# Performance work log

Measured on AMD Instinct MI355X. Metric: run time of the kernel, lower is better.

## Reference

```python
import jax, jax.numpy as jnp
import numpy as np

EPS = 1e-6
NEG_SLOPE = 0.2
B, C, E, F = 8, 2048, 256, 256


def setup_inputs() -> dict:
    key = jax.random.key(0)
    k1, k2, k3, k4, k5, k6 = jax.random.split(key, 6)
    X = jax.random.normal(k1, (B, C, E, 3), dtype=jnp.float32)
    J = jax.random.normal(k2, (B, C, E, 3), dtype=jnp.float32)
    A = jax.random.normal(k3, (F, E), dtype=jnp.float32)
    Bw = jax.random.normal(k4, (F, E), dtype=jnp.float32)
    Cw = jax.random.normal(k5, (F, E), dtype=jnp.float32)
    # VNLeakyReLU map_to_dir weight [F, F] (nn.Linear-style scale)
    W = jax.random.normal(k6, (F, F), dtype=jnp.float32) / jnp.sqrt(jnp.float32(F))
    return {"X": X, "J": J, "A": A, "Bw": Bw, "Cw": Cw, "W": W}


def _basis(J):
    # normalized direction [B,C,E,3]
    nJ = J / (jnp.linalg.norm(J, axis=-1, keepdims=True) + EPS)
    sub = nJ[..., :2]                                   # [B,C,E,2]
    Uz = -(sub * sub).sum(-1) / (nJ[..., 2] + EPS)      # [B,C,E]
    U = jnp.concatenate([sub, Uz[..., None]], axis=-1)  # [B,C,E,3]
    nU = U / (jnp.linalg.norm(U, axis=-1, keepdims=True) + EPS)
    nV = jnp.cross(nU, nJ)                              # [B,C,E,3]
    # rows of R are (U, V, J): R[..., i, j] matches torch reshape of cat
    return jnp.stack([nU, nV, nJ], axis=-2)             # [B,C,E,3,3]


def reference(X, J, A, Bw, Cw, W):
    R = _basis(J)                                        # [B,C,E,3,3]
    RT = jnp.swapaxes(R, -1, -2)                         # [B,C,E,3,3]
    # rtx[..., i] = RT[..., i, :] . X  (per torch get_rtx)
    rtx = jnp.einsum('bceij,bcej->bcei', RT, X)          # [B,C,E,3]

    def rrtx(i, r):
        # indexed_R = R[..., :, i]; broadcast-multiply by scalar field r
        return R[..., :, i] * r[..., None]               # [B,C,E,3]

    a = rrtx(0, rtx[..., 0]) + rrtx(1, rtx[..., 1])
    b = rrtx(1, rtx[..., 0]) - rrtx(0, rtx[..., 1])
    c = rrtx(2, rtx[..., 2])
    Y = (jnp.einsum('fe,bcei->bcfi', A, a)
         + jnp.einsum('fe,bcei->bcfi', Bw, b)
         + jnp.einsum('fe,bcei->bcfi', Cw, c))           # [B,C,F,3]

    x = jnp.transpose(Y, (0, 2, 3, 1))                   # [B,F,3,C]
    # VNLeakyReLU: direction d via linear over feature dim
    d = jnp.einsum('fg,bgic->bfic', W, x)                # [B,F,3,C]
    dot = (x * d).sum(axis=2, keepdims=True)             # [B,F,1,C]
    mask = (dot >= 0).astype(x.dtype)
    dns = (d * d).sum(axis=2, keepdims=True)
    x_out = (NEG_SLOPE * x
             + (1.0 - NEG_SLOPE) * (mask * x
                                    + (1.0 - mask) * (x - dot / (dns + EPS) * d)))
    return x_out
```

## Files before the change

### kernel.cpp

```cpp
#include <hip/hip_runtime.h>


constexpr float EPSf  = 1e-6f;
constexpr int Bdim = 8, Cdim = 2048, Edim = 256, Fdim = 256;
constexpr int NT  = 16;
constexpr int KC1 = 24;
constexpr int KC2 = 8;
constexpr int ZLD = 776;
constexpr int YLD = 264;
constexpr int M_ROWS = KC1 * 16 * 64;
constexpr int W_ROWS = KC2 * 16 * 64;

typedef __attribute__((ext_vector_type(8))) _Float16 half8;
typedef __attribute__((ext_vector_type(4))) _Float16 half4;
typedef __attribute__((ext_vector_type(4))) float    f32x4;

__device__ __forceinline__ void basis_abc(float Xx, float Xy, float Xz,
                                          float Jx, float Jy, float Jz,
                                          float* a, float* bb, float* cc)
{
    const float jn  = sqrtf(Jx*Jx + Jy*Jy + Jz*Jz) + EPSf;
    const float rj  = 1.0f / jn;
    const float nJx = Jx * rj, nJy = Jy * rj, nJz = Jz * rj;
    const float h   = nJx*nJx + nJy*nJy;
    const float Uz  = -h / (nJz + EPSf);
    const float un  = sqrtf(h + Uz*Uz) + EPSf;
    const float ru  = 1.0f / un;
    const float nUx = nJx * ru, nUy = nJy * ru, nUz = Uz * ru;
    const float nVx = nUy*nJz - nUz*nJy;
    const float nVy = nUz*nJx - nUx*nJz;
    const float nVz = nUx*nJy - nUy*nJx;
    const float r0 = nUx*Xx + nVx*Xy + nJx*Xz;
    const float r1 = nUy*Xx + nVy*Xy + nJy*Xz;
    const float r2 = nUz*Xx + nVz*Xy + nJz*Xz;
    a[0]  = nUx*r0 + nUy*r1;   a[1]  = nVx*r0 + nVy*r1;   a[2]  = nJx*r0 + nJy*r1;
    bb[0] = nUy*r0 - nUx*r1;   bb[1] = nVy*r0 - nVx*r1;   bb[2] = nJy*r0 - nJx*r1;
    cc[0] = nUz*r2;            cc[1] = nVz*r2;            cc[2] = nJz*r2;
}

__global__ __launch_bounds__(256)
void prep_weights_f16(const float* __restrict__ Ap, const float* __restrict__ Bp,
                      const float* __restrict__ Cp, const float* __restrict__ Wp,
                      _Float16* __restrict__ ws)
{
    const int tid = blockIdx.x * 256 + threadIdx.x;
    const bool isW = tid >= M_ROWS;
    const int row = isW ? tid - M_ROWS : tid;
    const int l   = row & 63;
    const int ft  = (row >> 6) & 15;
    const int kc  = row >> 10;
    const int f   = ft * 16 + (l & 15);
    const int k0  = kc * 32 + ((l >> 4) << 3);

    const float* src;
    int e0;
    if (isW)            { src = Wp; e0 = k0; }
    else if (k0 < 256)  { src = Ap; e0 = k0; }
    else if (k0 < 512)  { src = Bp; e0 = k0 - 256; }
    else                { src = Cp; e0 = k0 - 512; }

    const float* p = src + f * 256 + e0;
    half8 v;
    #pragma unroll
    for (int j = 0; j < 8; ++j) v[j] = (_Float16)p[j];

    _Float16* dst = ws + (isW ? (size_t)M_ROWS * 8 : 0);
    *reinterpret_cast<half8*>(dst + (size_t)row * 8) = v;
}

__global__ __launch_bounds__(512, 4)
void fused_mfma_f16(const float* __restrict__ Xp, const float* __restrict__ Jp,
                    const _Float16* __restrict__ wsM, const _Float16* __restrict__ wsW,
                    float* __restrict__ outp)
{
    __shared__ __align__(16) _Float16 lds[48 * ZLD];

    const int t  = threadIdx.x;
    const int s0 = blockIdx.x * NT;
    const int b  = s0 >> 11;
    const int c0 = s0 & (Cdim - 1);

    {
        const int equad = t & 63;
        const int sq    = t >> 6;
        const int e0    = equad * 4;
        #pragma unroll
        for (int ss = 0; ss < 2; ++ss) {
            const int s = sq * 2 + ss;
            const long site = (long)(b * Cdim + c0 + s);
            const float4* X4 = reinterpret_cast<const float4*>(Xp) + site * 192 + equad * 3;
            const float4* J4 = reinterpret_cast<const float4*>(Jp) + site * 192 + equad * 3;
            const float4 xA = X4[0], xB = X4[1], xC = X4[2];
            const float4 jA = J4[0], jB = J4[1], jC = J4[2];
            const float xf[12] = {xA.x,xA.y,xA.z,xA.w, xB.x,xB.y,xB.z,xB.w, xC.x,xC.y,xC.z,xC.w};
            const float jf[12] = {jA.x,jA.y,jA.z,jA.w, jB.x,jB.y,jB.z,jB.w, jC.x,jC.y,jC.z,jC.w};

            half4 za[3], zb[3], zc[3];
            #pragma unroll
            for (int ee = 0; ee < 4; ++ee) {
                float a[3], bb[3], cc[3];
                basis_abc(xf[3*ee], xf[3*ee+1], xf[3*ee+2],
                          jf[3*ee], jf[3*ee+1], jf[3*ee+2], a, bb, cc);
                #pragma unroll
                for (int i = 0; i < 3; ++i) {
                    za[i][ee] = (_Float16)a[i];
                    zb[i][ee] = (_Float16)bb[i];
                    zc[i][ee] = (_Float16)cc[i];
                }
            }
            #pragma unroll
            for (int i = 0; i < 3; ++i) {
                _Float16* rowp = &lds[(i * NT + s) * ZLD];
                *reinterpret_cast<half4*>(rowp +       e0) = za[i];
                *reinterpret_cast<half4*>(rowp + 256 + e0) = zb[i];
                *reinterpret_cast<half4*>(rowp + 512 + e0) = zc[i];
            }
        }
    }
    __syncthreads();

    const int wid = t >> 6;
    const int l   = t & 63;
    const int lr  = l & 15;
    const int lk  = (l >> 4) * 8;

    f32x4 Yacc[2][3];
    #pragma unroll
    for (int q = 0; q < 2; ++q)
        #pragma unroll
        for (int nt = 0; nt < 3; ++nt)
            Yacc[q][nt] = f32x4{0.f, 0.f, 0.f, 0.f};

    const half8* Mf = reinterpret_cast<const half8*>(wsM);
    for (int kc = 0; kc < KC1; ++kc) {
        half8 af[2];
        #pragma unroll
        for (int q = 0; q < 2; ++q)
            af[q] = Mf[(kc * 16 + wid * 2 + q) * 64 + l];
        half8 zf[3];
        #pragma unroll
        for (int nt = 0; nt < 3; ++nt)
            zf[nt] = *reinterpret_cast<const half8*>(&lds[(nt * NT + lr) * ZLD + kc * 32 + lk]);
        #pragma unroll
        for (int q = 0; q < 2; ++q)
            #pragma unroll
            for (int nt = 0; nt < 3; ++nt)
                Yacc[q][nt] = __builtin_amdgcn_mfma_f32_16x16x32_f16(af[q], zf[nt], Yacc[q][nt], 0, 0, 0);
    }
    __syncthreads();

    #pragma unroll
    for (int q = 0; q < 2; ++q) {
        const int row = (wid * 2 + q) * 16 + (l >> 4) * 4;
        #pragma unroll
        for (int nt = 0; nt < 3; ++nt) {
            const int col = nt * NT + lr;
            half4 v = { (_Float16)Yacc[q][nt][0], (_Float16)Yacc[q][nt][1],
                        (_Float16)Yacc[q][nt][2], (_Float16)Yacc[q][nt][3] };
            *reinterpret_cast<half4*>(&lds[col * YLD + row]) = v;
        }
    }
    __syncthreads();

    f32x4 Dacc[2][3];
    #pragma unroll
    for (int q = 0; q < 2; ++q)
        #pragma unroll
        for (int nt = 0; nt < 3; ++nt)
            Dacc[q][nt] = f32x4{0.f, 0.f, 0.f, 0.f};

    const half8* Wf = reinterpret_cast<const half8*>(wsW);
    for (int kc = 0; kc < KC2; ++kc) {
        half8 af[2];
        #pragma unroll
        for (int q = 0; q < 2; ++q)
            af[q] = Wf[(kc * 16 + wid * 2 + q) * 64 + l];
        half8 yf[3];
        #pragma unroll
        for (int nt = 0; nt < 3; ++nt)
            yf[nt] = *reinterpret_cast<const half8*>(&lds[(nt * NT + lr) * YLD + kc * 32 + lk]);
        #pragma unroll
        for (int q = 0; q < 2; ++q)
            #pragma unroll
            for (int nt = 0; nt < 3; ++nt)
                Dacc[q][nt] = __builtin_amdgcn_mfma_f32_16x16x32_f16(af[q], yf[nt], Dacc[q][nt], 0, 0, 0);
    }

    #pragma unroll
    for (int q = 0; q < 2; ++q) {
        const int fbase = (wid * 2 + q) * 16 + (l >> 4) * 4;
        #pragma unroll
        for (int r = 0; r < 4; ++r) {
#pragma clang fp contract(off)
            const float x0 = Yacc[q][0][r], x1 = Yacc[q][1][r], x2 = Yacc[q][2][r];
            const float d0 = Dacc[q][0][r], d1 = Dacc[q][1][r], d2 = Dacc[q][2][r];
            const float dot = (x0*d0 + x1*d1) + x2*d2;
            const float dns = (d0*d0 + d1*d1) + d2*d2;
            const float sc  = dot / (dns + EPSf);
            const bool  pos = (dot >= 0.f);
            const int f = fbase + r;
            const long obase = ((long)(b * Fdim + f) * 3) * Cdim + c0 + lr;
            const float c0v = pos ? x0 : (x0 - sc*d0);
            const float c1v = pos ? x1 : (x1 - sc*d1);
            const float c2v = pos ? x2 : (x2 - sc*d2);
            outp[obase + 0 * Cdim] = 0.2f*x0 + 0.8f*c0v;
            outp[obase + 1 * Cdim] = 0.2f*x1 + 0.8f*c1v;
            outp[obase + 2 * Cdim] = 0.2f*x2 + 0.8f*c2v;
        }
    }
}

__device__ __forceinline__ float comp(const float4& v, int k) {
    return k == 0 ? v.x : k == 1 ? v.y : k == 2 ? v.z : v.w;
}

__global__ __launch_bounds__(256)
void fused_cl_lrelu_fp32(const float* __restrict__ Xp, const float* __restrict__ Jp,
                         const float* __restrict__ Ap, const float* __restrict__ Bp,
                         const float* __restrict__ Cp, const float* __restrict__ Wp,
                         float* __restrict__ outp)
{
    __shared__ float4 sabc[4 * Edim * 3];
    __shared__ float  ylds[4 * 3][Fdim];

    const int t   = threadIdx.x;
    const int s0  = blockIdx.x * 4;
    const int b   = s0 / Cdim;
    const int c0  = s0 % Cdim;

    #pragma unroll
    for (int r = 0; r < 4; ++r) {
        const int e  = t;
        const int idx = ((b * Cdim + c0 + r) * Edim + e) * 3;
        float a[3], bb[3], cc[3];
        basis_abc(Xp[idx], Xp[idx+1], Xp[idx+2], Jp[idx], Jp[idx+1], Jp[idx+2], a, bb, cc);
        const int base = (r * Edim + e) * 3;
        sabc[base + 0] = make_float4(a[0], a[1], a[2], bb[0]);
        sabc[base + 1] = make_float4(bb[1], bb[2], cc[0], cc[1]);
        sabc[base + 2] = make_float4(cc[2], 0.f, 0.f, 0.f);
    }
    __syncthreads();

    const int fl = t & 63;
    const int cg = t >> 6;
    float Y[4][3];
    #pragma unroll
    for (int q = 0; q < 4; ++q) Y[q][0] = Y[q][1] = Y[q][2] = 0.f;

    const float4* A4 = reinterpret_cast<const float4*>(Ap);
    const float4* B4 = reinterpret_cast<const float4*>(Bp);
    const float4* C4 = reinterpret_cast<const float4*>(Cp);
    for (int e4 = 0; e4 < Edim / 4; ++e4) {
        float4 wa[4], wb[4], wc[4];
        #pragma unroll
        for (int q = 0; q < 4; ++q) {
            const int f = q * 64 + fl;
            wa[q] = A4[f * (Edim/4) + e4];
            wb[q] = B4[f * (Edim/4) + e4];
            wc[q] = C4[f * (Edim/4) + e4];
        }
        #pragma unroll
        for (int k = 0; k < 4; ++k) {
            const int e = e4 * 4 + k;
            const float4 p0 = sabc[(cg * Edim + e) * 3 + 0];
            const float4 p1 = sabc[(cg * Edim + e) * 3 + 1];
            const float4 p2 = sabc[(cg * Edim + e) * 3 + 2];
            #pragma unroll
            for (int q = 0; q < 4; ++q) {
                const float Af = comp(wa[q], k), Bf = comp(wb[q], k), Cf = comp(wc[q], k);
                Y[q][0] += Af * p0.x + Bf * p0.w + Cf * p1.z;
                Y[q][1] += Af * p0.y + Bf * p1.x + Cf * p1.w;
                Y[q][2] += Af * p0.z + Bf * p1.y + Cf * p2.x;
            }
        }
    }
    #pragma unroll
    for (int q = 0; q < 4; ++q) {
        const int f = q * 64 + fl;
        ylds[cg * 3 + 0][f] = Y[q][0];
        ylds[cg * 3 + 1][f] = Y[q][1];
        ylds[cg * 3 + 2][f] = Y[q][2];
    }
    __syncthreads();

    float D[4][3];
    #pragma unroll
    for (int q = 0; q < 4; ++q) D[q][0] = D[q][1] = D[q][2] = 0.f;
    const float4* W4 = reinterpret_cast<const float4*>(Wp);
    for (int g4 = 0; g4 < Fdim / 4; ++g4) {
        float4 ww[4];
        #pragma unroll
        for (int q = 0; q < 4; ++q) ww[q] = W4[(q * 64 + fl) * (Fdim/4) + g4];
        const float4 y0 = *reinterpret_cast<const float4*>(&ylds[cg * 3 + 0][g4 * 4]);
        const float4 y1 = *reinterpret_cast<const float4*>(&ylds[cg * 3 + 1][g4 * 4]);
        const float4 y2 = *reinterpret_cast<const float4*>(&ylds[cg * 3 + 2][g4 * 4]);
        #pragma unroll
        for (int k = 0; k < 4; ++k) {
            #pragma unroll
            for (int q = 0; q < 4; ++q) {
                const float Wv = comp(ww[q], k);
                D[q][0] += Wv * comp(y0, k);
                D[q][1] += Wv * comp(y1, k);
                D[q][2] += Wv * comp(y2, k);
            }
        }
    }

    float* outl = reinterpret_cast<float*>(sabc);
    #pragma unroll
    for (int q = 0; q < 4; ++q) {
        const int f = q * 64 + fl;
        const float dot = (Y[q][0]*D[q][0] + Y[q][1]*D[q][1]) + Y[q][2]*D[q][2];
        const float dns = (D[q][0]*D[q][0] + D[q][1]*D[q][1]) + D[q][2]*D[q][2];
        const float s   = dot / (dns + EPSf);
        const bool  pos = (dot >= 0.f);
        #pragma unroll
        for (int i = 0; i < 3; ++i) {
            const float x = Y[q][i], d = D[q][i];
            outl[(f * 3 + i) * 4 + cg] = 0.2f*x + 0.8f*(pos ? x : x - s*d);
        }
    }
    __syncthreads();
    const float4* o4 = reinterpret_cast<const float4*>(outl);
    float4* O4 = reinterpret_cast<float4*>(outp);
    const int c4 = c0 >> 2;
    #pragma unroll
    for (int i = 0; i < 3; ++i)
        O4[((b * Fdim + t) * 3 + i) * (Cdim / 4) + c4] = o4[t * 3 + i];
}

extern "C" void kernel_launch(void* const* d_in, const int* in_sizes, int n_in,
                              void* d_out, int out_size, void* d_ws, size_t ws_size,
                              hipStream_t stream) {
    const float* X  = (const float*)d_in[0];
    const float* J  = (const float*)d_in[1];
    const float* A  = (const float*)d_in[2];
    const float* Bw = (const float*)d_in[3];
    const float* Cw = (const float*)d_in[4];
    const float* W  = (const float*)d_in[5];
    float* out = (float*)d_out;

    constexpr size_t WS_NEED = (size_t)(M_ROWS + W_ROWS) * 8 * sizeof(_Float16);
    if (ws_size >= WS_NEED) {
        _Float16* wsM = (_Float16*)d_ws;
        _Float16* wsW = wsM + (size_t)M_ROWS * 8;
        prep_weights_f16<<<(M_ROWS + W_ROWS) / 256, 256, 0, stream>>>(A, Bw, Cw, W, wsM);
        fused_mfma_f16<<<Bdim * Cdim / NT, 512, 0, stream>>>(X, J, wsM, wsW, out);
    } else {
        fused_cl_lrelu_fp32<<<Bdim * Cdim / 4, 256, 0, stream>>>(X, J, A, Bw, Cw, W, out);
    }
}
```

Baseline: 60.40 us.

## Persist blocks over four site groups with double-buffered basis prefetch

Each block now processes four 16-site groups in sequence with 1024 threads (16 waves, one 16-row F tile per wave instead of two). The next group's X/J are loaded into registers during the current group's GEMMs, and its basis values are written into the alternate LDS buffer after the epilogue. The aim is to hide global load latency behind MFMA work and cut the number of blocks launched. In exchange, LDS use doubles, each wave gets less MFMA work per weight fragment load, and the large block size may reduce occupancy.

```diff
diff --git a/kernel.cpp b/kernel.cpp
--- a/kernel.cpp
+++ b/kernel.cpp
@@ -8,6 +8,8 @@
 constexpr int KC2 = 8;
 constexpr int ZLD = 776;
 constexpr int YLD = 264;
+constexpr int ZSZ = 48 * ZLD;
+constexpr int GROUPS = 4;
 constexpr int M_ROWS = KC1 * 16 * 64;
 constexpr int W_ROWS = KC2 * 16 * 64;
 
@@ -68,145 +70,146 @@
     *reinterpret_cast<half8*>(dst + (size_t)row * 8) = v;
 }
 
-__global__ __launch_bounds__(512, 4)
+__global__ __launch_bounds__(1024, 4)
 void fused_mfma_f16(const float* __restrict__ Xp, const float* __restrict__ Jp,
                     const _Float16* __restrict__ wsM, const _Float16* __restrict__ wsW,
                     float* __restrict__ outp)
 {
-    __shared__ __align__(16) _Float16 lds[48 * ZLD];
-
-    const int t  = threadIdx.x;
-    const int s0 = blockIdx.x * NT;
-    const int b  = s0 >> 11;
-    const int c0 = s0 & (Cdim - 1);
-
-    {
-        const int equad = t & 63;
-        const int sq    = t >> 6;
-        const int e0    = equad * 4;
-        #pragma unroll
-        for (int ss = 0; ss < 2; ++ss) {
-            const int s = sq * 2 + ss;
-            const long site = (long)(b * Cdim + c0 + s);
-            const float4* X4 = reinterpret_cast<const float4*>(Xp) + site * 192 + equad * 3;
-            const float4* J4 = reinterpret_cast<const float4*>(Jp) + site * 192 + equad * 3;
-            const float4 xA = X4[0], xB = X4[1], xC = X4[2];
-            const float4 jA = J4[0], jB = J4[1], jC = J4[2];
-            const float xf[12] = {xA.x,xA.y,xA.z,xA.w, xB.x,xB.y,xB.z,xB.w, xC.x,xC.y,xC.z,xC.w};
-            const float jf[12] = {jA.x,jA.y,jA.z,jA.w, jB.x,jB.y,jB.z,jB.w, jC.x,jC.y,jC.z,jC.w};
-
-            half4 za[3], zb[3], zc[3];
-            #pragma unroll
-            for (int ee = 0; ee < 4; ++ee) {
-                float a[3], bb[3], cc[3];
-                basis_abc(xf[3*ee], xf[3*ee+1], xf[3*ee+2],
-                          jf[3*ee], jf[3*ee+1], jf[3*ee+2], a, bb, cc);
-                #pragma unroll
-                for (int i = 0; i < 3; ++i) {
-                    za[i][ee] = (_Float16)a[i];
-                    zb[i][ee] = (_Float16)bb[i];
-                    zc[i][ee] = (_Float16)cc[i];
-                }
-            }
+    __shared__ __align__(16) _Float16 lds[2 * ZSZ];
+
+    const int t     = threadIdx.x;
+    const int site  = t >> 6;
+    const int equad = t & 63;
+    const int e0    = equad * 4;
+    const int wid   = site;
+    const int l     = t & 63;
+    const int lr    = l & 15;
+    const int lk    = (l >> 4) * 8;
+    const int g0    = blockIdx.x * GROUPS;
+
+    float4 xv[3], jv[3];
+
+    auto LOADIN = [&](int g) {
+        const long sg = (long)(g0 + g) * NT + site;
+        const float4* X4 = reinterpret_cast<const float4*>(Xp) + sg * 192 + equad * 3;
+        const float4* J4 = reinterpret_cast<const float4*>(Jp) + sg * 192 + equad * 3;
+        xv[0] = X4[0]; xv[1] = X4[1]; xv[2] = X4[2];
+        jv[0] = J4[0]; jv[1] = J4[1]; jv[2] = J4[2];
+    };
+
+    auto BASIS_STORE = [&](int g) {
+        _Float16* Z = lds + (g & 1) * ZSZ;
+        const float xf[12] = {xv[0].x,xv[0].y,xv[0].z,xv[0].w,
+                              xv[1].x,xv[1].y,xv[1].z,xv[1].w,
+                              xv[2].x,xv[2].y,xv[2].z,xv[2].w};
+        const float jf[12] = {jv[0].x,jv[0].y,jv[0].z,jv[0].w,
+                              jv[1].x,jv[1].y,jv[1].z,jv[1].w,
+                              jv[2].x,jv[2].y,jv[2].z,jv[2].w};
+        half4 za[3], zb[3], zc[3];
+        #pragma unroll
+        for (int ee = 0; ee < 4; ++ee) {
+            float a[3], bb[3], cc[3];
+            basis_abc(xf[3*ee], xf[3*ee+1], xf[3*ee+2],
+                      jf[3*ee], jf[3*ee+1], jf[3*ee+2], a, bb, cc);
             #pragma unroll
             for (int i = 0; i < 3; ++i) {
-                _Float16* rowp = &lds[(i * NT + s) * ZLD];
-                *reinterpret_cast<half4*>(rowp +       e0) = za[i];
-                *reinterpret_cast<half4*>(rowp + 256 + e0) = zb[i];
-                *reinterpret_cast<half4*>(rowp + 512 + e0) = zc[i];
-            }
-        }
-    }
+                za[i][ee] = (_Float16)a[i];
+                zb[i][ee] = (_Float16)bb[i];
+                zc[i][ee] = (_Float16)cc[i];
+            }
+        }
+        #pragma unroll
+        for (int i = 0; i < 3; ++i) {
+            _Float16* rowp = Z + (i * NT + site) * ZLD;
+            *reinterpret_cast<half4*>(rowp +       e0) = za[i];
+            *reinterpret_cast<half4*>(rowp + 256 + e0) = zb[i];
+            *reinterpret_cast<half4*>(rowp + 512 + e0) = zc[i];
+        }
+    };
+
+    LOADIN(0);
+    BASIS_STORE(0);
     __syncthreads();
 
-    const int wid = t >> 6;
-    const int l   = t & 63;
-    const int lr  = l & 15;
-    const int lk  = (l >> 4) * 8;
-
-    f32x4 Yacc[2][3];
-    #pragma unroll
-    for (int q = 0; q < 2; ++q)
-        #pragma unroll
-        for (int nt = 0; nt < 3; ++nt)
-            Yacc[q][nt] = f32x4{0.f, 0.f, 0.f, 0.f};
-
     const half8* Mf = reinterpret_cast<const half8*>(wsM);
-    for (int kc = 0; kc < KC1; ++kc) {
-        half8 af[2];
-        #pragma unroll
-        for (int q = 0; q < 2; ++q)
-            af[q] = Mf[(kc * 16 + wid * 2 + q) * 64 + l];
-        half8 zf[3];
-        #pragma unroll
-        for (int nt = 0; nt < 3; ++nt)
-            zf[nt] = *reinterpret_cast<const half8*>(&lds[(nt * NT + lr) * ZLD + kc * 32 + lk]);
-        #pragma unroll
-        for (int q = 0; q < 2; ++q)
+    const half8* Wf = reinterpret_cast<const half8*>(wsW);
+
+    for (int g = 0; g < GROUPS; ++g) {
+        const _Float16* Z = lds + (g & 1) * ZSZ;
+
+        if (g + 1 < GROUPS) LOADIN(g + 1);
+
+        f32x4 Yacc[3];
+        #pragma unroll
+        for (int nt = 0; nt < 3; ++nt) Yacc[nt] = f32x4{0.f, 0.f, 0.f, 0.f};
+
+        for (int kc = 0; kc < KC1; ++kc) {
+            half8 af = Mf[(kc * 16 + wid) * 64 + l];
+            half8 zf[3];
             #pragma unroll
             for (int nt = 0; nt < 3; ++nt)
-                Yacc[q][nt] = __builtin_amdgcn_mfma_f32_16x16x32_f16(af[q], zf[nt], Yacc[q][nt], 0, 0, 0);
-    }
-    __syncthreads();
-
-    #pragma unroll
-    for (int q = 0; q < 2; ++q) {
-        const int row = (wid * 2 + q) * 16 + (l >> 4) * 4;
-        #pragma unroll
-        for (int nt = 0; nt < 3; ++nt) {
-            const int col = nt * NT + lr;
-            half4 v = { (_Float16)Yacc[q][nt][0], (_Float16)Yacc[q][nt][1],
-                        (_Float16)Yacc[q][nt][2], (_Float16)Yacc[q][nt][3] };
-            *reinterpret_cast<half4*>(&lds[col * YLD + row]) = v;
-        }
-    }
-    __syncthreads();
-
-    f32x4 Dacc[2][3];
-    #pragma unroll
-    for (int q = 0; q < 2; ++q)
-        #pragma unroll
-        for (int nt = 0; nt < 3; ++nt)
-            Dacc[q][nt] = f32x4{0.f, 0.f, 0.f, 0.f};
-
-    const half8* Wf = reinterpret_cast<const half8*>(wsW);
-    for (int kc = 0; kc < KC2; ++kc) {
-        half8 af[2];
-        #pragma unroll
-        for (int q = 0; q < 2; ++q)
-            af[q] = Wf[(kc * 16 + wid * 2 + q) * 64 + l];
-        half8 yf[3];
-        #pragma unroll
-        for (int nt = 0; nt < 3; ++nt)
-            yf[nt] = *reinterpret_cast<const half8*>(&lds[(nt * NT + lr) * YLD + kc * 32 + lk]);
-        #pragma unroll
-        for (int q = 0; q < 2; ++q)
+                zf[nt] = *reinterpret_cast<const half8*>(&Z[(nt * NT + lr) * ZLD + kc * 32 + lk]);
             #pragma unroll
             for (int nt = 0; nt < 3; ++nt)
-                Dacc[q][nt] = __builtin_amdgcn_mfma_f32_16x16x32_f16(af[q], yf[nt], Dacc[q][nt], 0, 0, 0);
-    }
-
-    #pragma unroll
-    for (int q = 0; q < 2; ++q) {
-        const int fbase = (wid * 2 + q) * 16 + (l >> 4) * 4;
-        #pragma unroll
-        for (int r = 0; r < 4; ++r) {
+                Yacc[nt] = __builtin_amdgcn_mfma_f32_16x16x32_f16(af, zf[nt], Yacc[nt], 0, 0, 0);
+        }
+        __syncthreads();
+
+        _Float16* Yt = lds + (g & 1) * ZSZ;
+        {
+            const int row = wid * 16 + (l >> 4) * 4;
+            #pragma unroll
+            for (int nt = 0; nt < 3; ++nt) {
+                const int col = nt * NT + lr;
+                half4 v = { (_Float16)Yacc[nt][0], (_Float16)Yacc[nt][1],
+                            (_Float16)Yacc[nt][2], (_Float16)Yacc[nt][3] };
+                *reinterpret_cast<half4*>(&Yt[col * YLD + row]) = v;
+            }
+        }
+        __syncthreads();
+
+        f32x4 Dacc[3];
+        #pragma unroll
+        for (int nt = 0; nt < 3; ++nt) Dacc[nt] = f32x4{0.f, 0.f, 0.f, 0.f};
+
+        for (int kc = 0; kc < KC2; ++kc) {
+            half8 wf = Wf[(kc * 16 + wid) * 64 + l];
+            half8 yf[3];
+            #pragma unroll
+            for (int nt = 0; nt < 3; ++nt)
+                yf[nt] = *reinterpret_cast<const half8*>(&Yt[(nt * NT + lr) * YLD + kc * 32 + lk]);
+            #pragma unroll
+            for (int nt = 0; nt < 3; ++nt)
+                Dacc[nt] = __builtin_amdgcn_mfma_f32_16x16x32_f16(wf, yf[nt], Dacc[nt], 0, 0, 0);
+        }
+
+        {
+            const int s0g   = (g0 + g) * NT;
+            const int b     = s0g >> 11;
+            const int c0    = s0g & (Cdim - 1);
+            const int fbase = wid * 16 + (l >> 4) * 4;
+            #pragma unroll
+            for (int r = 0; r < 4; ++r) {
 #pragma clang fp contract(off)
-            const float x0 = Yacc[q][0][r], x1 = Yacc[q][1][r], x2 = Yacc[q][2][r];
-            const float d0 = Dacc[q][0][r], d1 = Dacc[q][1][r], d2 = Dacc[q][2][r];
-            const float dot = (x0*d0 + x1*d1) + x2*d2;
-            const float dns = (d0*d0 + d1*d1) + d2*d2;
-            const float sc  = dot / (dns + EPSf);
-            const bool  pos = (dot >= 0.f);
-            const int f = fbase + r;
-            const long obase = ((long)(b * Fdim + f) * 3) * Cdim + c0 + lr;
-            const float c0v = pos ? x0 : (x0 - sc*d0);
-            const float c1v = pos ? x1 : (x1 - sc*d1);
-            const float c2v = pos ? x2 : (x2 - sc*d2);
-            outp[obase + 0 * Cdim] = 0.2f*x0 + 0.8f*c0v;
-            outp[obase + 1 * Cdim] = 0.2f*x1 + 0.8f*c1v;
-            outp[obase + 2 * Cdim] = 0.2f*x2 + 0.8f*c2v;
-        }
+                const float x0 = Yacc[0][r], x1 = Yacc[1][r], x2 = Yacc[2][r];
+                const float d0 = Dacc[0][r], d1 = Dacc[1][r], d2 = Dacc[2][r];
+                const float dot = (x0*d0 + x1*d1) + x2*d2;
+                const float dns = (d0*d0 + d1*d1) + d2*d2;
+                const float sc  = dot / (dns + EPSf);
+                const bool  pos = (dot >= 0.f);
+                const int f = fbase + r;
+                const long obase = ((long)(b * Fdim + f) * 3) * Cdim + c0 + lr;
+                const float c0v = pos ? x0 : (x0 - sc*d0);
+                const float c1v = pos ? x1 : (x1 - sc*d1);
+                const float c2v = pos ? x2 : (x2 - sc*d2);
+                outp[obase + 0 * Cdim] = 0.2f*x0 + 0.8f*c0v;
+                outp[obase + 1 * Cdim] = 0.2f*x1 + 0.8f*c1v;
+                outp[obase + 2 * Cdim] = 0.2f*x2 + 0.8f*c2v;
+            }
+        }
+
+        if (g + 1 < GROUPS) BASIS_STORE(g + 1);
+        __syncthreads();
     }
 }
 
@@ -345,7 +348,7 @@
         _Float16* wsM = (_Float16*)d_ws;
         _Float16* wsW = wsM + (size_t)M_ROWS * 8;
         prep_weights_f16<<<(M_ROWS + W_ROWS) / 256, 256, 0, stream>>>(A, Bw, Cw, W, wsM);
-        fused_mfma_f16<<<Bdim * Cdim / NT, 512, 0, stream>>>(X, J, wsM, wsW, out);
+        fused_mfma_f16<<<Bdim * Cdim / NT / GROUPS, 1024, 0, stream>>>(X, J, wsM, wsW, out);
     } else {
         fused_cl_lrelu_fp32<<<Bdim * Cdim / 4, 256, 0, stream>>>(X, J, A, Bw, Cw, W, out);
     }
```

After: 133.7 us. 121% more time.

## Halve sites per block and pack 24 component rows into two MFMA tiles

Applied to the files above, without the earlier changes.

Each block now handles 8 sites instead of 16, so 24 rows (3 components × 8 sites) fit in two 16-wide MFMA N-tiles instead of three. This halves the LDS footprint and accumulator registers, and the launch bound asks for 8 blocks per CU to raise occupancy. The cross-component dot products are rebuilt with xor-8 lane shuffles. In exchange, the weight fragments are reloaded from global memory twice as often per site, and the second tile wastes its 8 padding rows of MFMA work.

```diff
diff --git a/kernel.cpp b/kernel.cpp
--- a/kernel.cpp
+++ b/kernel.cpp
@@ -3,11 +3,12 @@
 
 constexpr float EPSf  = 1e-6f;
 constexpr int Bdim = 8, Cdim = 2048, Edim = 256, Fdim = 256;
-constexpr int NT  = 16;
+constexpr int NT  = 8;
 constexpr int KC1 = 24;
 constexpr int KC2 = 8;
 constexpr int ZLD = 776;
 constexpr int YLD = 264;
+constexpr int NROWS = 24;
 constexpr int M_ROWS = KC1 * 16 * 64;
 constexpr int W_ROWS = KC2 * 16 * 64;
 
@@ -68,53 +69,49 @@
     *reinterpret_cast<half8*>(dst + (size_t)row * 8) = v;
 }
 
-__global__ __launch_bounds__(512, 4)
+__global__ __launch_bounds__(512, 8)
 void fused_mfma_f16(const float* __restrict__ Xp, const float* __restrict__ Jp,
                     const _Float16* __restrict__ wsM, const _Float16* __restrict__ wsW,
                     float* __restrict__ outp)
 {
-    __shared__ __align__(16) _Float16 lds[48 * ZLD];
+    __shared__ __align__(16) _Float16 lds[NROWS * ZLD];
 
     const int t  = threadIdx.x;
-    const int s0 = blockIdx.x * NT;
-    const int b  = s0 >> 11;
-    const int c0 = s0 & (Cdim - 1);
+    const long s0 = (long)blockIdx.x * NT;
+    const int b  = (int)(s0 >> 11);
+    const int c0 = (int)(s0 & (Cdim - 1));
 
     {
+        const int site  = t >> 6;
         const int equad = t & 63;
-        const int sq    = t >> 6;
         const int e0    = equad * 4;
-        #pragma unroll
-        for (int ss = 0; ss < 2; ++ss) {
-            const int s = sq * 2 + ss;
-            const long site = (long)(b * Cdim + c0 + s);
-            const float4* X4 = reinterpret_cast<const float4*>(Xp) + site * 192 + equad * 3;
-            const float4* J4 = reinterpret_cast<const float4*>(Jp) + site * 192 + equad * 3;
-            const float4 xA = X4[0], xB = X4[1], xC = X4[2];
-            const float4 jA = J4[0], jB = J4[1], jC = J4[2];
-            const float xf[12] = {xA.x,xA.y,xA.z,xA.w, xB.x,xB.y,xB.z,xB.w, xC.x,xC.y,xC.z,xC.w};
-            const float jf[12] = {jA.x,jA.y,jA.z,jA.w, jB.x,jB.y,jB.z,jB.w, jC.x,jC.y,jC.z,jC.w};
-
-            half4 za[3], zb[3], zc[3];
-            #pragma unroll
-            for (int ee = 0; ee < 4; ++ee) {
-                float a[3], bb[3], cc[3];
-                basis_abc(xf[3*ee], xf[3*ee+1], xf[3*ee+2],
-                          jf[3*ee], jf[3*ee+1], jf[3*ee+2], a, bb, cc);
-                #pragma unroll
-                for (int i = 0; i < 3; ++i) {
-                    za[i][ee] = (_Float16)a[i];
-                    zb[i][ee] = (_Float16)bb[i];
-                    zc[i][ee] = (_Float16)cc[i];
-                }
-            }
+        const long sg   = s0 + site;
+        const float4* X4 = reinterpret_cast<const float4*>(Xp) + sg * 192 + equad * 3;
+        const float4* J4 = reinterpret_cast<const float4*>(Jp) + sg * 192 + equad * 3;
+        const float4 xA = X4[0], xB = X4[1], xC = X4[2];
+        const float4 jA = J4[0], jB = J4[1], jC = J4[2];
+        const float xf[12] = {xA.x,xA.y,xA.z,xA.w, xB.x,xB.y,xB.z,xB.w, xC.x,xC.y,xC.z,xC.w};
+        const float jf[12] = {jA.x,jA.y,jA.z,jA.w, jB.x,jB.y,jB.z,jB.w, jC.x,jC.y,jC.z,jC.w};
+
+        half4 za[3], zb[3], zc[3];
+        #pragma unroll
+        for (int ee = 0; ee < 4; ++ee) {
+            float a[3], bb[3], cc[3];
+            basis_abc(xf[3*ee], xf[3*ee+1], xf[3*ee+2],
+                      jf[3*ee], jf[3*ee+1], jf[3*ee+2], a, bb, cc);
             #pragma unroll
             for (int i = 0; i < 3; ++i) {
-                _Float16* rowp = &lds[(i * NT + s) * ZLD];
-                *reinterpret_cast<half4*>(rowp +       e0) = za[i];
-                *reinterpret_cast<half4*>(rowp + 256 + e0) = zb[i];
-                *reinterpret_cast<half4*>(rowp + 512 + e0) = zc[i];
-            }
+                za[i][ee] = (_Float16)a[i];
+                zb[i][ee] = (_Float16)bb[i];
+                zc[i][ee] = (_Float16)cc[i];
+            }
+        }
+        #pragma unroll
+        for (int i = 0; i < 3; ++i) {
+            _Float16* rowp = &lds[(i * NT + site) * ZLD];
+            *reinterpret_cast<half4*>(rowp +       e0) = za[i];
+            *reinterpret_cast<half4*>(rowp + 256 + e0) = zb[i];
+            *reinterpret_cast<half4*>(rowp + 512 + e0) = zc[i];
         }
     }
     __syncthreads();
@@ -122,14 +119,18 @@
     const int wid = t >> 6;
     const int l   = t & 63;
     const int lr  = l & 15;
-    const int lk  = (l >> 4) * 8;
-
-    f32x4 Yacc[2][3];
+    const int hi  = l >> 4;
+    const int lk  = hi * 8;
+
+    f32x4 Yacc[2][2];
     #pragma unroll
     for (int q = 0; q < 2; ++q)
         #pragma unroll
-        for (int nt = 0; nt < 3; ++nt)
+        for (int nt = 0; nt < 2; ++nt)
             Yacc[q][nt] = f32x4{0.f, 0.f, 0.f, 0.f};
+
+    const int zr0 = lr;
+    const int zr1 = (16 + lr < NROWS) ? (16 + lr) : 0;
 
     const half8* Mf = reinterpret_cast<const half8*>(wsM);
     for (int kc = 0; kc < KC1; ++kc) {
@@ -137,75 +138,81 @@
         #pragma unroll
         for (int q = 0; q < 2; ++q)
             af[q] = Mf[(kc * 16 + wid * 2 + q) * 64 + l];
-        half8 zf[3];
-        #pragma unroll
-        for (int nt = 0; nt < 3; ++nt)
-            zf[nt] = *reinterpret_cast<const half8*>(&lds[(nt * NT + lr) * ZLD + kc * 32 + lk]);
-        #pragma unroll
-        for (int q = 0; q < 2; ++q)
-            #pragma unroll
-            for (int nt = 0; nt < 3; ++nt)
-                Yacc[q][nt] = __builtin_amdgcn_mfma_f32_16x16x32_f16(af[q], zf[nt], Yacc[q][nt], 0, 0, 0);
+        half8 zf0 = *reinterpret_cast<const half8*>(&lds[zr0 * ZLD + kc * 32 + lk]);
+        half8 zf1 = *reinterpret_cast<const half8*>(&lds[zr1 * ZLD + kc * 32 + lk]);
+        #pragma unroll
+        for (int q = 0; q < 2; ++q) {
+            Yacc[q][0] = __builtin_amdgcn_mfma_f32_16x16x32_f16(af[q], zf0, Yacc[q][0], 0, 0, 0);
+            Yacc[q][1] = __builtin_amdgcn_mfma_f32_16x16x32_f16(af[q], zf1, Yacc[q][1], 0, 0, 0);
+        }
     }
     __syncthreads();
 
     #pragma unroll
     for (int q = 0; q < 2; ++q) {
-        const int row = (wid * 2 + q) * 16 + (l >> 4) * 4;
-        #pragma unroll
-        for (int nt = 0; nt < 3; ++nt) {
-            const int col = nt * NT + lr;
-            half4 v = { (_Float16)Yacc[q][nt][0], (_Float16)Yacc[q][nt][1],
-                        (_Float16)Yacc[q][nt][2], (_Float16)Yacc[q][nt][3] };
-            *reinterpret_cast<half4*>(&lds[col * YLD + row]) = v;
-        }
-    }
-    __syncthreads();
-
-    f32x4 Dacc[2][3];
+        const int gcol = (wid * 2 + q) * 16 + hi * 4;
+        #pragma unroll
+        for (int nt = 0; nt < 2; ++nt) {
+            const int row = nt * 16 + lr;
+            if (row < NROWS) {
+                half4 v = { (_Float16)Yacc[q][nt][0], (_Float16)Yacc[q][nt][1],
+                            (_Float16)Yacc[q][nt][2], (_Float16)Yacc[q][nt][3] };
+                *reinterpret_cast<half4*>(&lds[row * YLD + gcol]) = v;
+            }
+        }
+    }
+    __syncthreads();
+
+    f32x4 Dacc[2][2];
     #pragma unroll
     for (int q = 0; q < 2; ++q)
         #pragma unroll
-        for (int nt = 0; nt < 3; ++nt)
+        for (int nt = 0; nt < 2; ++nt)
             Dacc[q][nt] = f32x4{0.f, 0.f, 0.f, 0.f};
 
     const half8* Wf = reinterpret_cast<const half8*>(wsW);
     for (int kc = 0; kc < KC2; ++kc) {
-        half8 af[2];
+        half8 wf[2];
         #pragma unroll
         for (int q = 0; q < 2; ++q)
-            af[q] = Wf[(kc * 16 + wid * 2 + q) * 64 + l];
-        half8 yf[3];
-        #pragma unroll
-        for (int nt = 0; nt < 3; ++nt)
-            yf[nt] = *reinterpret_cast<const half8*>(&lds[(nt * NT + lr) * YLD + kc * 32 + lk]);
-        #pragma unroll
-        for (int q = 0; q < 2; ++q)
-            #pragma unroll
-            for (int nt = 0; nt < 3; ++nt)
-                Dacc[q][nt] = __builtin_amdgcn_mfma_f32_16x16x32_f16(af[q], yf[nt], Dacc[q][nt], 0, 0, 0);
-    }
-
+            wf[q] = Wf[(kc * 16 + wid * 2 + q) * 64 + l];
+        half8 yf0 = *reinterpret_cast<const half8*>(&lds[zr0 * YLD + kc * 32 + lk]);
+        half8 yf1 = *reinterpret_cast<const half8*>(&lds[zr1 * YLD + kc * 32 + lk]);
+        #pragma unroll
+        for (int q = 0; q < 2; ++q) {
+            Dacc[q][0] = __builtin_amdgcn_mfma_f32_16x16x32_f16(wf[q], yf0, Dacc[q][0], 0, 0, 0);
+            Dacc[q][1] = __builtin_amdgcn_mfma_f32_16x16x32_f16(wf[q], yf1, Dacc[q][1], 0, 0, 0);
+        }
+    }
+
+    const int s   = lr & 7;
+    const bool lo = (lr < 8);
     #pragma unroll
     for (int q = 0; q < 2; ++q) {
-        const int fbase = (wid * 2 + q) * 16 + (l >> 4) * 4;
+        const int fbase = (wid * 2 + q) * 16 + hi * 4;
         #pragma unroll
         for (int r = 0; r < 4; ++r) {
 #pragma clang fp contract(off)
-            const float x0 = Yacc[q][0][r], x1 = Yacc[q][1][r], x2 = Yacc[q][2][r];
-            const float d0 = Dacc[q][0][r], d1 = Dacc[q][1][r], d2 = Dacc[q][2][r];
-            const float dot = (x0*d0 + x1*d1) + x2*d2;
-            const float dns = (d0*d0 + d1*d1) + d2*d2;
+            const float xt0 = Yacc[q][0][r], dt0 = Dacc[q][0][r];
+            const float xt1 = Yacc[q][1][r], dt1 = Dacc[q][1][r];
+            const float p0  = xt0 * dt0;
+            const float p0s = p0 + __shfl_xor(p0, 8);
+            const float p1o = __shfl_xor(xt1 * dt1, 8);
+            const float dot = p0s + (lo ? xt1 * dt1 : p1o);
+            const float q0  = dt0 * dt0;
+            const float q0s = q0 + __shfl_xor(q0, 8);
+            const float q1o = __shfl_xor(dt1 * dt1, 8);
+            const float dns = q0s + (lo ? dt1 * dt1 : q1o);
             const float sc  = dot / (dns + EPSf);
             const bool  pos = (dot >= 0.f);
             const int f = fbase + r;
-            const long obase = ((long)(b * Fdim + f) * 3) * Cdim + c0 + lr;
-            const float c0v = pos ? x0 : (x0 - sc*d0);
-            const float c1v = pos ? x1 : (x1 - sc*d1);
-            const float c2v = pos ? x2 : (x2 - sc*d2);
-            outp[obase + 0 * Cdim] = 0.2f*x0 + 0.8f*c0v;
-            outp[obase + 1 * Cdim] = 0.2f*x1 + 0.8f*c1v;
-            outp[obase + 2 * Cdim] = 0.2f*x2 + 0.8f*c2v;
+            const long obase = ((long)(b * Fdim + f) * 3) * Cdim + c0 + s;
+            const float v0 = 0.2f*xt0 + 0.8f*(pos ? xt0 : xt0 - sc*dt0);
+            outp[obase + (lo ? 0 : 1) * Cdim] = v0;
+            if (lo) {
+                const float v2 = 0.2f*xt1 + 0.8f*(pos ? xt1 : xt1 - sc*dt1);
+                outp[obase + 2 * Cdim] = v2;
+            }
         }
     }
 }
```

Result: slower. 90.32 us (+49.5%).
